# Kernel tuning notes

Measured on AMD Instinct MI355X. Metric: run time of the kernel, lower is better.

The kernel has to match this reference:

```python
import jax, jax.numpy as jnp
import numpy as np

EMBED_DIM = 1024


def setup_inputs() -> dict:
    key = jax.random.key(0)
    ks = jax.random.split(key, 9)
    d = EMBED_DIM
    s = 1.0 / np.sqrt(d)
    return {
        "x": jax.random.normal(ks[0], (4, 2048, d), dtype=jnp.float32),
        "wq": jax.random.normal(ks[1], (d, d), dtype=jnp.float32) * s,
        "bq": jnp.zeros((d,), dtype=jnp.float32),
        "wk": jax.random.normal(ks[2], (d, d), dtype=jnp.float32) * s,
        "bk": jnp.zeros((d,), dtype=jnp.float32),
        "wv": jax.random.normal(ks[3], (d, d), dtype=jnp.float32) * s,
        "bv": jnp.zeros((d,), dtype=jnp.float32),
        "wo": jax.random.normal(ks[4], (d, d), dtype=jnp.float32) * s,
        "bo": jnp.zeros((d,), dtype=jnp.float32),
    }


def reference(x, wq, bq, wk, bk, wv, bv, wo, bo):
    # x: [B, S, D]; weights stored as [D_in, D_out] (torch Linear applies x @ W.T,
    # here we fold the transpose into storage).
    d = x.shape[-1]
    q = x @ wq + bq
    k = x @ wk + bk
    v = x @ wv + bv
    scores = jnp.einsum('bqd,bkd->bqk', q, k) / jnp.sqrt(jnp.float32(d))
    attn = jax.nn.softmax(scores, axis=-1)
    out = jnp.einsum('bqk,bkd->bqd', attn, v)
    return out @ wo + bo
```

## Files before the change

kernel.cpp:

```cpp
#include <hip/hip_runtime.h>
#include <stdint.h>

typedef __attribute__((ext_vector_type(4))) float f32x4;
typedef __attribute__((ext_vector_type(8))) short short8v;
typedef __attribute__((ext_vector_type(4))) unsigned short ushort4v;
typedef __attribute__((ext_vector_type(8))) unsigned short ushort8v;

__device__ __forceinline__ unsigned short f2b(float x) {
  union { float f; unsigned int u; } c; c.f = x;
  unsigned int r = (c.u + 0x7fffu + ((c.u >> 16) & 1u)) >> 16;
  return (unsigned short)r;
}

__device__ __forceinline__ float b2f(unsigned short x) {
  union { unsigned int u; float f; } c; c.u = ((unsigned int)x) << 16;
  return c.f;
}

__device__ __forceinline__ void gload_lds16(const void* g, void* l) {
  __builtin_amdgcn_global_load_lds(
      (const __attribute__((address_space(1))) void*)g,
      (__attribute__((address_space(3))) void*)l, 16, 0, 0);
}

__device__ __forceinline__ f32x4 MFMA16(short8v a, short8v b, f32x4 c) {
  return __builtin_amdgcn_mfma_f32_16x16x32_bf16(a, b, c, 0, 0, 0);
}

template <int N>
__device__ __forceinline__ void wvm() {
  if constexpr (N == 8) asm volatile("s_waitcnt vmcnt(8)" ::: "memory");
  else if constexpr (N == 6) asm volatile("s_waitcnt vmcnt(6)" ::: "memory");
  else if constexpr (N == 4) asm volatile("s_waitcnt vmcnt(4)" ::: "memory");
  else if constexpr (N == 3) asm volatile("s_waitcnt vmcnt(3)" ::: "memory");
  else asm volatile("s_waitcnt vmcnt(0)" ::: "memory");
}

__global__ __launch_bounds__(256) void prep(
    const float* __restrict__ x, const float* __restrict__ w0,
    const float* __restrict__ w1, const float* __restrict__ w2,
    const float* __restrict__ w3, unsigned short* __restrict__ xb,
    unsigned short* __restrict__ o0, unsigned short* __restrict__ o1,
    unsigned short* __restrict__ o2, unsigned short* __restrict__ o3) {
  const int z = blockIdx.z;
  if (z == 4) {
    const int linear = blockIdx.y * 16 + blockIdx.x;
    for (int i = linear * 256 + threadIdx.x; i < 1048576; i += 65536) {
      f32x4 a = *((const f32x4*)x + (size_t)i * 2);
      f32x4 b = *((const f32x4*)x + (size_t)i * 2 + 1);
      ushort8v o;
      o[0] = f2b(a[0]); o[1] = f2b(a[1]); o[2] = f2b(a[2]); o[3] = f2b(a[3]);
      o[4] = f2b(b[0]); o[5] = f2b(b[1]); o[6] = f2b(b[2]); o[7] = f2b(b[3]);
      *((ushort8v*)xb + i) = o;
    }
    return;
  }
  const float* W = z == 0 ? w0 : z == 1 ? w1 : z == 2 ? w2 : w3;
  unsigned short* WT = z == 0 ? o0 : z == 1 ? o1 : z == 2 ? o2 : o3;
  __shared__ float t[64][65];
  const int bi = blockIdx.y * 64, bj = blockIdx.x * 64;
#pragma unroll
  for (int i = 0; i < 16; ++i) {
    int idx = i * 256 + threadIdx.x;
    int r = idx >> 6, c = idx & 63;
    t[r][c] = W[(size_t)(bi + r) * 1024 + bj + c];
  }
  __syncthreads();
#pragma unroll
  for (int i = 0; i < 16; ++i) {
    int idx = i * 256 + threadIdx.x;
    int r = idx >> 6, c = idx & 63;
    WT[(size_t)(bj + r) * 1024 + bi + c] = f2b(t[c][r]);
  }
}

__global__ __launch_bounds__(256) void softmax_bf16(unsigned short* __restrict__ S,
                                                    long long bstride) {
  unsigned short* row = S + (long long)blockIdx.y * bstride + (size_t)blockIdx.x * 2048;
  const int t = threadIdx.x;
  ushort8v u = *((const ushort8v*)row + t);
  float v[8];
#pragma unroll
  for (int j = 0; j < 8; ++j) v[j] = b2f(u[j]);
  float m = v[0];
#pragma unroll
  for (int j = 1; j < 8; ++j) m = fmaxf(m, v[j]);
#pragma unroll
  for (int o = 32; o; o >>= 1) m = fmaxf(m, __shfl_xor(m, o));
  __shared__ float red[4];
  const int wid = t >> 6, lane = t & 63;
  if (lane == 0) red[wid] = m;
  __syncthreads();
  m = fmaxf(fmaxf(red[0], red[1]), fmaxf(red[2], red[3]));
  float s = 0.f;
#pragma unroll
  for (int j = 0; j < 8; ++j) { v[j] = __expf(v[j] - m); s += v[j]; }
#pragma unroll
  for (int o = 32; o; o >>= 1) s += __shfl_xor(s, o);
  __syncthreads();
  if (lane == 0) red[wid] = s;
  __syncthreads();
  s = red[0] + red[1] + red[2] + red[3];
  const float inv = 1.f / s;
  ushort8v o8;
#pragma unroll
  for (int j = 0; j < 8; ++j) o8[j] = f2b(v[j] * inv);
  *((ushort8v*)row + t) = o8;
}

__global__ __launch_bounds__(256) void softmax_rows(float* __restrict__ S,
                                                    long long bstride) {
  float* row = S + (long long)blockIdx.y * bstride + (size_t)blockIdx.x * 2048;
  const int t = threadIdx.x;
  f32x4 a = *(const f32x4*)(row + t * 8);
  f32x4 b = *(const f32x4*)(row + t * 8 + 4);
  float m = fmaxf(fmaxf(fmaxf(a[0], a[1]), fmaxf(a[2], a[3])),
                  fmaxf(fmaxf(b[0], b[1]), fmaxf(b[2], b[3])));
#pragma unroll
  for (int o = 32; o; o >>= 1) m = fmaxf(m, __shfl_xor(m, o));
  __shared__ float red[4];
  const int wid = t >> 6, lane = t & 63;
  if (lane == 0) red[wid] = m;
  __syncthreads();
  m = fmaxf(fmaxf(red[0], red[1]), fmaxf(red[2], red[3]));
  float e[8];
  float s = 0.f;
#pragma unroll
  for (int j = 0; j < 4; ++j) { e[j] = __expf(a[j] - m); s += e[j]; }
#pragma unroll
  for (int j = 0; j < 4; ++j) { e[4 + j] = __expf(b[j] - m); s += e[4 + j]; }
#pragma unroll
  for (int o = 32; o; o >>= 1) s += __shfl_xor(s, o);
  __syncthreads();
  if (lane == 0) red[wid] = s;
  __syncthreads();
  s = red[0] + red[1] + red[2] + red[3];
  const float inv = 1.f / s;
  ushort8v o8;
#pragma unroll
  for (int j = 0; j < 8; ++j) o8[j] = f2b(e[j] * inv);
  __syncthreads();
  *((ushort8v*)row + t) = o8;
}

template <int EPI, int BM>
__global__ __launch_bounds__(512, 2) void gemm256(
    const unsigned short* __restrict__ A, int lda,
    const unsigned short* __restrict__ B, int ldb,
    void* __restrict__ C0, void* __restrict__ C1, void* __restrict__ C2,
    int ldc, const float* __restrict__ bias0, const float* __restrict__ bias1,
    const float* __restrict__ bias2, float scale, int K,
    long long bsA, long long bsB, long long bsC) {
  extern __shared__ __align__(16) char smem[];
  constexpr int ABY = BM * 64;
  constexpr int KHS = ABY + 16384;
  constexpr int SBUF = 2 * KHS;
  constexpr int MF = BM / 32;
  constexpr int FH = MF / 2;
  constexpr int AL = BM / 128;
  constexpr int L = AL + 2;

  const int tid = threadIdx.x;
  const int z = blockIdx.z;
  A += (long long)z * bsA;
  B += (long long)z * bsB;
  const int blkrow = blockIdx.y * BM, blkcol = blockIdx.x * 256;
  const int lane = tid & 63, wid = tid >> 6;
  const int kblk = lane >> 4, l15 = lane & 15;
  const int arw = (wid >> 2) * (BM / 2) + l15;
  const int brw = (wid & 3) * 64 + l15;
  const int aoff = arw * 64 + ((kblk ^ ((arw >> 1) & 3)) << 4);
  const int boff = ABY + brw * 64 + ((kblk ^ ((brw >> 1) & 3)) << 4);
  const int srow = tid >> 2;
  const int scc = (((tid & 3) ^ ((srow >> 1) & 3)) << 3);
  const unsigned short* ag = A + (size_t)(blkrow + srow) * lda + scc;
  const unsigned short* bg = B + (size_t)(blkcol + srow) * ldb + scc;

  auto stA = [&](char* buf, int kt, int kh) {
    const unsigned short* g = ag + kt * 64 + kh * 32;
    char* l = buf + kh * KHS + tid * 16;
#pragma unroll
    for (int rr = 0; rr < AL; ++rr)
      gload_lds16(g + (size_t)(rr * 128) * lda, l + rr * 8192);
  };
  auto stB = [&](char* buf, int kt, int kh) {
    const unsigned short* g = bg + kt * 64 + kh * 32;
    char* l = buf + ABY + kh * KHS + tid * 16;
    gload_lds16(g, l);
    gload_lds16(g + (size_t)128 * ldb, l + 8192);
  };

  f32x4 acc[MF][4] = {};
  short8v af[4], bf[4];

#define LDAH(BUF, KK, MB)                                                     \
  { _Pragma("unroll") for (int m_ = 0; m_ < FH; ++m_)                         \
      af[m_] = *(const short8v*)((BUF) + (KK)*KHS + aoff + ((MB) + m_) * 1024); }
#define LDB4(BUF, KK)                                                         \
  { _Pragma("unroll") for (int n_ = 0; n_ < 4; ++n_)                          \
      bf[n_] = *(const short8v*)((BUF) + (KK)*KHS + boff + n_ * 1024); }
#define MMH(MH)                                                               \
  { _Pragma("unroll") for (int m_ = 0; m_ < FH; ++m_)                         \
      _Pragma("unroll") for (int n_ = 0; n_ < 4; ++n_)                        \
        acc[(MH)*FH + m_][n_] = MFMA16(af[m_], bf[n_], acc[(MH)*FH + m_][n_]); }
#define BAR __builtin_amdgcn_s_barrier()
#define WLGKM0 asm volatile("s_waitcnt lgkmcnt(0)" ::: "memory")

  const int NT = K >> 6;
  stA(smem, 0, 0); stB(smem, 0, 0); stA(smem, 0, 1); stB(smem, 0, 1);
  wvm<L>();
  BAR;
  for (int t = 0; t < NT; ++t) {
    char* cur = smem + (t & 1) * SBUF;
    char* nxt = smem + ((t + 1) & 1) * SBUF;
    const bool pf = (t + 1 < NT);
    LDAH(cur, 0, 0);
    LDB4(cur, 0);
    if (pf) { stA(nxt, t + 1, 0); stB(nxt, t + 1, 0); }
    BAR; WLGKM0;
    __builtin_amdgcn_s_setprio(1);
    MMH(0);
    __builtin_amdgcn_s_setprio(0);
    BAR;
    LDAH(cur, 0, FH);
    if (pf) { stA(nxt, t + 1, 1); stB(nxt, t + 1, 1); }
    BAR; WLGKM0;
    __builtin_amdgcn_s_setprio(1);
    MMH(1);
    __builtin_amdgcn_s_setprio(0);
    if (pf) wvm<2 * L>(); else wvm<0>();
    BAR;
    LDAH(cur, 1, 0);
    LDB4(cur, 1);
    BAR; WLGKM0;
    __builtin_amdgcn_s_setprio(1);
    MMH(0);
    __builtin_amdgcn_s_setprio(0);
    BAR;
    LDAH(cur, 1, FH);
    BAR; WLGKM0;
    __builtin_amdgcn_s_setprio(1);
    MMH(1);
    __builtin_amdgcn_s_setprio(0);
    if (pf) wvm<L>();
    BAR;
  }

  const int gr0 = blkrow + (wid >> 2) * (BM / 2) + kblk * 4;
  const int gc0 = blkcol + (wid & 3) * 64 + l15;
  if (EPI == 0) {
    float* C = (float*)C0 + (long long)z * bsC;
#pragma unroll
    for (int mi = 0; mi < MF; ++mi)
#pragma unroll
      for (int n = 0; n < 4; ++n) {
        const int gc = gc0 + n * 16;
        const float badd = bias0 ? bias0[gc] : 0.f;
#pragma unroll
        for (int j = 0; j < 4; ++j)
          C[(size_t)(gr0 + mi * 16 + j) * ldc + gc] = acc[mi][n][j] * scale + badd;
      }
  } else if (EPI == 1) {
    unsigned short* C = (unsigned short*)C0 + (long long)z * bsC;
#pragma unroll
    for (int mi = 0; mi < MF; ++mi)
#pragma unroll
      for (int n = 0; n < 4; ++n) {
        const int gc = gc0 + n * 16;
        const float badd = bias0 ? bias0[gc] : 0.f;
#pragma unroll
        for (int j = 0; j < 4; ++j)
          C[(size_t)(gr0 + mi * 16 + j) * ldc + gc] = f2b(acc[mi][n][j] * scale + badd);
      }
  } else if (EPI == 2) {
    const int seg = blkcol >> 10;
    unsigned short* O = (unsigned short*)(seg == 0 ? C0 : C1);
    const float* bb = (seg == 0 ? bias0 : bias1);
#pragma unroll
    for (int mi = 0; mi < MF; ++mi)
#pragma unroll
      for (int n = 0; n < 4; ++n) {
        const int lc = gc0 + n * 16 - seg * 1024;
        const float badd = bb[lc];
#pragma unroll
        for (int j = 0; j < 4; ++j)
          O[(size_t)(gr0 + mi * 16 + j) * 1024 + lc] = f2b(acc[mi][n][j] + badd);
      }
  } else {
    unsigned short* O = (unsigned short*)C2;
#pragma unroll
    for (int mi = 0; mi < MF; ++mi)
#pragma unroll
      for (int n = 0; n < 4; ++n) {
        const int gc = gc0 + n * 16;
        const float badd = bias2[gc];
        ushort4v pk;
#pragma unroll
        for (int j = 0; j < 4; ++j) pk[j] = f2b(acc[mi][n][j] + badd);
        *(ushort4v*)(O + (size_t)gc * 8192 + gr0 + mi * 16) = pk;
      }
  }
#undef LDAH
#undef LDB4
#undef MMH
#undef BAR
#undef WLGKM0
}

template <int OMODE, bool BIAS, bool SCALE>
__global__ __launch_bounds__(256, 2) void gemm_bt(
    const unsigned short* __restrict__ A, int lda,
    const unsigned short* __restrict__ B, int ldb,
    void* __restrict__ Cp, int ldc,
    const float* __restrict__ bias, float scale, int K,
    long long bsA, long long bsB, long long bsC) {
  __shared__ unsigned short As[128 * 32];
  __shared__ unsigned short Bs[128 * 32];
  const int tid = threadIdx.x;
  A += (long long)blockIdx.z * bsA;
  B += (long long)blockIdx.z * bsB;
  const int brow = blockIdx.y * 128, bcol = blockIdx.x * 128;
  const int wid = tid >> 6, lane = tid & 63;
  const int wr = (wid >> 1) * 64, wc = (wid & 1) * 64;
  const int lrow = lane & 15, kblk = lane >> 4;
  f32x4 acc[4][4] = {};
  for (int kk = 0; kk < K; kk += 32) {
#pragma unroll
    for (int r = 0; r < 2; ++r) {
      int idx = r * 256 + tid;
      int row = idx >> 2, seg = (idx & 3) * 8;
      gload_lds16(A + (size_t)(brow + row) * lda + kk + seg, (char*)As + idx * 16);
      gload_lds16(B + (size_t)(bcol + row) * ldb + kk + seg, (char*)Bs + idx * 16);
    }
    __syncthreads();
    short8v af[4], bv[4];
#pragma unroll
    for (int m = 0; m < 4; ++m)
      af[m] = *(const short8v*)(As + (wr + m * 16 + lrow) * 32 + kblk * 8);
#pragma unroll
    for (int n = 0; n < 4; ++n)
      bv[n] = *(const short8v*)(Bs + (wc + n * 16 + lrow) * 32 + kblk * 8);
#pragma unroll
    for (int m = 0; m < 4; ++m)
#pragma unroll
      for (int n = 0; n < 4; ++n)
        acc[m][n] = MFMA16(af[m], bv[n], acc[m][n]);
    __syncthreads();
  }
  const int r0 = brow + wr + kblk * 4;
  const int c0 = bcol + wc + lrow;
  if (OMODE == 0) {
    float* C = (float*)Cp + (long long)blockIdx.z * bsC;
#pragma unroll
    for (int m = 0; m < 4; ++m)
#pragma unroll
      for (int n = 0; n < 4; ++n) {
        const int cc = c0 + n * 16;
        const float badd = BIAS ? bias[cc] : 0.f;
#pragma unroll
        for (int j = 0; j < 4; ++j) {
          float v = acc[m][n][j];
          if (SCALE) v *= scale;
          C[(size_t)(r0 + m * 16 + j) * ldc + cc] = v + badd;
        }
      }
  } else if (OMODE == 1) {
    unsigned short* C = (unsigned short*)Cp + (long long)blockIdx.z * bsC;
#pragma unroll
    for (int m = 0; m < 4; ++m)
#pragma unroll
      for (int n = 0; n < 4; ++n) {
        const int cc = c0 + n * 16;
        const float badd = BIAS ? bias[cc] : 0.f;
#pragma unroll
        for (int j = 0; j < 4; ++j) {
          float v = acc[m][n][j];
          if (SCALE) v *= scale;
          C[(size_t)(r0 + m * 16 + j) * ldc + cc] = f2b(v + badd);
        }
      }
  } else {
    unsigned short* C = (unsigned short*)Cp + (long long)blockIdx.z * bsC;
#pragma unroll
    for (int m = 0; m < 4; ++m)
#pragma unroll
      for (int n = 0; n < 4; ++n) {
        const int cc = c0 + n * 16;
        const float badd = BIAS ? bias[cc] : 0.f;
        ushort4v pk;
#pragma unroll
        for (int j = 0; j < 4; ++j) {
          float v = acc[m][n][j];
          if (SCALE) v *= scale;
          pk[j] = f2b(v + badd);
        }
        *(ushort4v*)(C + (size_t)cc * ldc + (r0 + m * 16)) = pk;
      }
  }
}

__global__ __launch_bounds__(256) void cvt_batch(const float* __restrict__ in,
                                                 unsigned short* __restrict__ out,
                                                 int n8) {
  for (int i = blockIdx.x * 256 + threadIdx.x; i < n8; i += gridDim.x * 256) {
    f32x4 a = *((const f32x4*)in + (size_t)i * 2);
    f32x4 b = *((const f32x4*)in + (size_t)i * 2 + 1);
    ushort8v o;
    o[0] = f2b(a[0]); o[1] = f2b(a[1]); o[2] = f2b(a[2]); o[3] = f2b(a[3]);
    o[4] = f2b(b[0]); o[5] = f2b(b[1]); o[6] = f2b(b[2]); o[7] = f2b(b[3]);
    *((ushort8v*)out + i) = o;
  }
}

extern "C" void kernel_launch(void* const* d_in, const int* in_sizes, int n_in,
                              void* d_out, int out_size, void* d_ws, size_t ws_size,
                              hipStream_t stream) {
  const float* x  = (const float*)d_in[0];
  const float* wq = (const float*)d_in[1];
  const float* bq = (const float*)d_in[2];
  const float* wk = (const float*)d_in[3];
  const float* bk = (const float*)d_in[4];
  const float* wv = (const float*)d_in[5];
  const float* bv = (const float*)d_in[6];
  const float* wo = (const float*)d_in[7];
  const float* bo = (const float*)d_in[8];
  float* out = (float*)d_out;
  char* ws = (char*)d_ws;

  const long long WELEM = 1024LL * 1024;
  const long long BATCH = 2048LL * 1024;
  const long long FULL  = 4 * BATCH;
  const long long SELEM = 2048LL * 2048;

  const size_t need_A = 8388608ull + 5ull * 16777216 + 4ull * 16777216;
  const size_t need_C = 8388608ull + 4ull * 4194304 + 16777216ull;

  if (ws_size >= need_A) {
    unsigned short* wqT = (unsigned short*)ws;
    unsigned short* wkT = wqT + WELEM;
    unsigned short* wvT = wkT + WELEM;
    unsigned short* woT = wvT + WELEM;
    unsigned short* xb  = woT + WELEM;
    unsigned short* qb  = xb + FULL;
    unsigned short* kb  = qb + FULL;
    unsigned short* vt  = kb + FULL;
    unsigned short* ao  = vt + FULL;
    unsigned short* S   = ao + FULL;

    hipFuncSetAttribute(reinterpret_cast<const void*>(&gemm256<2, 128>),
                        hipFuncAttributeMaxDynamicSharedMemorySize, 98304);
    hipFuncSetAttribute(reinterpret_cast<const void*>(&gemm256<3, 128>),
                        hipFuncAttributeMaxDynamicSharedMemorySize, 98304);
    hipFuncSetAttribute(reinterpret_cast<const void*>(&gemm256<1, 128>),
                        hipFuncAttributeMaxDynamicSharedMemorySize, 98304);
    hipFuncSetAttribute(reinterpret_cast<const void*>(&gemm256<0, 128>),
                        hipFuncAttributeMaxDynamicSharedMemorySize, 98304);

    prep<<<dim3(16, 16, 5), 256, 0, stream>>>(x, wq, wk, wv, wo, xb,
                                              wqT, wkT, wvT, woT);

    gemm256<2, 128><<<dim3(8, 64, 1), 512, 98304, stream>>>(
        xb, 1024, wqT, 1024, qb, kb, nullptr, 0, bq, bk, nullptr,
        1.f, 1024, 0, 0, 0);
    gemm256<3, 128><<<dim3(4, 64, 1), 512, 98304, stream>>>(
        xb, 1024, wvT, 1024, nullptr, nullptr, vt, 0, nullptr, nullptr, bv,
        1.f, 1024, 0, 0, 0);
    gemm256<1, 128><<<dim3(8, 16, 4), 512, 98304, stream>>>(
        qb, 1024, kb, 1024, S, nullptr, nullptr, 2048, nullptr, nullptr,
        nullptr, 0.03125f, 1024, BATCH, BATCH, SELEM);
    softmax_bf16<<<dim3(2048, 4), 256, 0, stream>>>(S, SELEM);
    gemm256<1, 128><<<dim3(4, 16, 4), 512, 98304, stream>>>(
        S, 2048, vt, 8192, ao, nullptr, nullptr, 1024, nullptr, nullptr,
        nullptr, 1.f, 2048, SELEM, 2048, BATCH);
    gemm256<0, 128><<<dim3(4, 64, 1), 512, 98304, stream>>>(
        ao, 1024, woT, 1024, out, nullptr, nullptr, 1024, bo, nullptr,
        nullptr, 1.f, 1024, 0, 0, 0);
  } else if (ws_size >= need_C) {
    unsigned short* wqT = (unsigned short*)ws;
    unsigned short* wkT = wqT + WELEM;
    unsigned short* wvT = wkT + WELEM;
    unsigned short* woT = wvT + WELEM;
    unsigned short* xb  = woT + WELEM;
    unsigned short* qb  = xb + BATCH;
    unsigned short* kb  = qb + BATCH;
    unsigned short* vtb = kb + BATCH;
    float* S = (float*)(vtb + BATCH);

    prep<<<dim3(16, 16, 4), 256, 0, stream>>>(x, wq, wk, wv, wo, xb,
                                              wqT, wkT, wvT, woT);

    for (int b = 0; b < 4; ++b) {
      cvt_batch<<<1024, 256, 0, stream>>>(x + b * BATCH, xb, (int)(BATCH / 8));
      dim3 gqkv(8, 16);
      gemm_bt<1, true, false><<<gqkv, 256, 0, stream>>>(xb, 1024, wqT, 1024, qb, 1024, bq, 1.f, 1024, 0, 0, 0);
      gemm_bt<1, true, false><<<gqkv, 256, 0, stream>>>(xb, 1024, wkT, 1024, kb, 1024, bk, 1.f, 1024, 0, 0, 0);
      gemm_bt<2, true, false><<<gqkv, 256, 0, stream>>>(xb, 1024, wvT, 1024, vtb, 2048, bv, 1.f, 1024, 0, 0, 0);
      gemm_bt<0, false, true><<<dim3(16, 16), 256, 0, stream>>>(
          qb, 1024, kb, 1024, S, 2048, nullptr, 0.03125f, 1024, 0, 0, 0);
      softmax_rows<<<dim3(2048, 1), 256, 0, stream>>>(S, 0);
      gemm_bt<1, false, false><<<dim3(8, 16), 256, 0, stream>>>(
          (const unsigned short*)S, 4096, vtb, 2048, xb, 1024, nullptr, 1.f, 2048, 0, 0, 0);
      gemm_bt<0, true, false><<<dim3(8, 16), 256, 0, stream>>>(
          xb, 1024, woT, 1024, out + b * BATCH, 1024, bo, 1.f, 1024, 0, 0, 0);
    }
  }
}
```

Baseline: 217.6 us.

## Add XCD-aware block swizzle, split fused QK projection, use 256-row tiles for scores

Adds a block-index remap so consecutive blocks sharing row panels land on the same XCD, which is meant to improve L2 reuse across the chiplets. It removes the fused Q/K epilogue and instead launches Q and K projections as separate GEMMs. It also switches the QK^T score GEMM to BM=256 tiles with 128KB of LDS, which raises per-block reuse but lowers occupancy and block count. The swizzle assumes the grid's y*z product divides by 8.

Result: no change. 213.8 us (-1.7%).

```diff
diff --git a/kernel.cpp b/kernel.cpp
--- a/kernel.cpp
+++ b/kernel.cpp
@@ -34,6 +34,19 @@
   else if constexpr (N == 4) asm volatile("s_waitcnt vmcnt(4)" ::: "memory");
   else if constexpr (N == 3) asm volatile("s_waitcnt vmcnt(3)" ::: "memory");
   else asm volatile("s_waitcnt vmcnt(0)" ::: "memory");
+}
+
+__device__ __forceinline__ void xcd_swz(int& ex, int& ey, int& ez) {
+  const int gx = gridDim.x, gy = gridDim.y, gz = gridDim.z;
+  const int lid = blockIdx.x + gx * (blockIdx.y + gy * blockIdx.z);
+  const int k = lid & 7;
+  const int j = lid >> 3;
+  const int lp = j / gx;
+  ex = j - lp * gx;
+  const int pe = (gy * gz) >> 3;
+  const int panel = k * pe + lp;
+  ey = panel % gy;
+  ez = panel / gy;
 }
 
 __global__ __launch_bounds__(256) void prep(
@@ -147,10 +160,8 @@
 __global__ __launch_bounds__(512, 2) void gemm256(
     const unsigned short* __restrict__ A, int lda,
     const unsigned short* __restrict__ B, int ldb,
-    void* __restrict__ C0, void* __restrict__ C1, void* __restrict__ C2,
-    int ldc, const float* __restrict__ bias0, const float* __restrict__ bias1,
-    const float* __restrict__ bias2, float scale, int K,
-    long long bsA, long long bsB, long long bsC) {
+    void* __restrict__ C0, int ldc, const float* __restrict__ bias0,
+    float scale, int K, long long bsA, long long bsB, long long bsC) {
   extern __shared__ __align__(16) char smem[];
   constexpr int ABY = BM * 64;
   constexpr int KHS = ABY + 16384;
@@ -161,10 +172,11 @@
   constexpr int L = AL + 2;
 
   const int tid = threadIdx.x;
-  const int z = blockIdx.z;
-  A += (long long)z * bsA;
-  B += (long long)z * bsB;
-  const int blkrow = blockIdx.y * BM, blkcol = blockIdx.x * 256;
+  int ex, ey, ez;
+  xcd_swz(ex, ey, ez);
+  A += (long long)ez * bsA;
+  B += (long long)ez * bsB;
+  const int blkrow = ey * BM, blkcol = ex * 256;
   const int lane = tid & 63, wid = tid >> 6;
   const int kblk = lane >> 4, l15 = lane & 15;
   const int arw = (wid >> 2) * (BM / 2) + l15;
@@ -249,7 +261,7 @@
   const int gr0 = blkrow + (wid >> 2) * (BM / 2) + kblk * 4;
   const int gc0 = blkcol + (wid & 3) * 64 + l15;
   if (EPI == 0) {
-    float* C = (float*)C0 + (long long)z * bsC;
+    float* C = (float*)C0 + (long long)ez * bsC;
 #pragma unroll
     for (int mi = 0; mi < MF; ++mi)
 #pragma unroll
@@ -261,7 +273,7 @@
           C[(size_t)(gr0 + mi * 16 + j) * ldc + gc] = acc[mi][n][j] * scale + badd;
       }
   } else if (EPI == 1) {
-    unsigned short* C = (unsigned short*)C0 + (long long)z * bsC;
+    unsigned short* C = (unsigned short*)C0 + (long long)ez * bsC;
 #pragma unroll
     for (int mi = 0; mi < MF; ++mi)
 #pragma unroll
@@ -272,28 +284,14 @@
         for (int j = 0; j < 4; ++j)
           C[(size_t)(gr0 + mi * 16 + j) * ldc + gc] = f2b(acc[mi][n][j] * scale + badd);
       }
-  } else if (EPI == 2) {
-    const int seg = blkcol >> 10;
-    unsigned short* O = (unsigned short*)(seg == 0 ? C0 : C1);
-    const float* bb = (seg == 0 ? bias0 : bias1);
-#pragma unroll
-    for (int mi = 0; mi < MF; ++mi)
-#pragma unroll
-      for (int n = 0; n < 4; ++n) {
-        const int lc = gc0 + n * 16 - seg * 1024;
-        const float badd = bb[lc];
-#pragma unroll
-        for (int j = 0; j < 4; ++j)
-          O[(size_t)(gr0 + mi * 16 + j) * 1024 + lc] = f2b(acc[mi][n][j] + badd);
-      }
   } else {
-    unsigned short* O = (unsigned short*)C2;
+    unsigned short* O = (unsigned short*)C0;
 #pragma unroll
     for (int mi = 0; mi < MF; ++mi)
 #pragma unroll
       for (int n = 0; n < 4; ++n) {
         const int gc = gc0 + n * 16;
-        const float badd = bias2[gc];
+        const float badd = bias0[gc];
         ushort4v pk;
 #pragma unroll
         for (int j = 0; j < 4; ++j) pk[j] = f2b(acc[mi][n][j] + badd);
@@ -447,34 +445,33 @@
     unsigned short* ao  = vt + FULL;
     unsigned short* S   = ao + FULL;
 
-    hipFuncSetAttribute(reinterpret_cast<const void*>(&gemm256<2, 128>),
+    hipFuncSetAttribute(reinterpret_cast<const void*>(&gemm256<1, 256>),
+                        hipFuncAttributeMaxDynamicSharedMemorySize, 131072);
+    hipFuncSetAttribute(reinterpret_cast<const void*>(&gemm256<1, 128>),
                         hipFuncAttributeMaxDynamicSharedMemorySize, 98304);
     hipFuncSetAttribute(reinterpret_cast<const void*>(&gemm256<3, 128>),
                         hipFuncAttributeMaxDynamicSharedMemorySize, 98304);
-    hipFuncSetAttribute(reinterpret_cast<const void*>(&gemm256<1, 128>),
-                        hipFuncAttributeMaxDynamicSharedMemorySize, 98304);
     hipFuncSetAttribute(reinterpret_cast<const void*>(&gemm256<0, 128>),
                         hipFuncAttributeMaxDynamicSharedMemorySize, 98304);
 
     prep<<<dim3(16, 16, 5), 256, 0, stream>>>(x, wq, wk, wv, wo, xb,
                                               wqT, wkT, wvT, woT);
 
-    gemm256<2, 128><<<dim3(8, 64, 1), 512, 98304, stream>>>(
-        xb, 1024, wqT, 1024, qb, kb, nullptr, 0, bq, bk, nullptr,
-        1.f, 1024, 0, 0, 0);
+    gemm256<1, 128><<<dim3(4, 64, 1), 512, 98304, stream>>>(
+        xb, 1024, wqT, 1024, qb, 1024, bq, 1.f, 1024, 0, 0, 0);
+    gemm256<1, 128><<<dim3(4, 64, 1), 512, 98304, stream>>>(
+        xb, 1024, wkT, 1024, kb, 1024, bk, 1.f, 1024, 0, 0, 0);
     gemm256<3, 128><<<dim3(4, 64, 1), 512, 98304, stream>>>(
-        xb, 1024, wvT, 1024, nullptr, nullptr, vt, 0, nullptr, nullptr, bv,
-        1.f, 1024, 0, 0, 0);
-    gemm256<1, 128><<<dim3(8, 16, 4), 512, 98304, stream>>>(
-        qb, 1024, kb, 1024, S, nullptr, nullptr, 2048, nullptr, nullptr,
-        nullptr, 0.03125f, 1024, BATCH, BATCH, SELEM);
+        xb, 1024, wvT, 1024, vt, 0, bv, 1.f, 1024, 0, 0, 0);
+    gemm256<1, 256><<<dim3(8, 8, 4), 512, 131072, stream>>>(
+        qb, 1024, kb, 1024, S, 2048, nullptr, 0.03125f, 1024,
+        BATCH, BATCH, SELEM);
     softmax_bf16<<<dim3(2048, 4), 256, 0, stream>>>(S, SELEM);
     gemm256<1, 128><<<dim3(4, 16, 4), 512, 98304, stream>>>(
-        S, 2048, vt, 8192, ao, nullptr, nullptr, 1024, nullptr, nullptr,
-        nullptr, 1.f, 2048, SELEM, 2048, BATCH);
+        S, 2048, vt, 8192, ao, 1024, nullptr, 1.f, 2048,
+        SELEM, 2048, BATCH);
     gemm256<0, 128><<<dim3(4, 64, 1), 512, 98304, stream>>>(
-        ao, 1024, woT, 1024, out, nullptr, nullptr, 1024, bo, nullptr,
-        nullptr, 1.f, 1024, 0, 0, 0);
+        ao, 1024, woT, 1024, out, 1024, bo, 1.f, 1024, 0, 0, 0);
   } else if (ws_size >= need_C) {
     unsigned short* wqT = (unsigned short*)ws;
     unsigned short* wkT = wqT + WELEM;
```
